# Kernel optimization log

Measured on AMD Instinct MI355X. Metric: run time of the kernel, lower is better.

## Reference

```python
import jax, jax.numpy as jnp
import numpy as np

N = 100000      # nodes
E = 1600000     # edges
D_IN = 128
D_H = 128
D_OUT = 128


def setup_inputs() -> dict:
    key = jax.random.key(0)
    k1, k2, k3, k4, k5, k6 = jax.random.split(key, 6)
    x = jax.random.normal(k1, (N, D_IN), dtype=jnp.float32)
    edge_index = jax.random.randint(k2, (2, E), 0, N, dtype=jnp.int32)
    # GCNConv params: glorot-ish scaled weights, zero bias (PyG default zeros bias)
    W1 = jax.random.normal(k3, (D_IN, D_H), dtype=jnp.float32) * (1.0 / np.sqrt(D_IN))
    b1 = jnp.zeros((D_H,), dtype=jnp.float32)
    W2 = jax.random.normal(k4, (D_H, D_OUT), dtype=jnp.float32) * (1.0 / np.sqrt(D_H))
    b2 = jnpps = jnp.zeros((D_OUT,), dtype=jnp.float32)
    return {"x": x, "edge_index": edge_index, "W1": W1, "b1": b1, "W2": W2, "b2": b2}


def _gcn_layer(x, edge_index, W, b):
    # PyG GCNConv with add_self_loops=True, symmetric normalization:
    # out = D^{-1/2} (A + I) D^{-1/2} (x W) + b, deg computed at target (col)
    n = x.shape[0]
    row, col = edge_index[0], edge_index[1]
    deg = jax.ops.segment_sum(jnp.ones(row.shape, dtype=x.dtype), col,
                              num_segments=n) + 1.0  # +1 for self-loop
    dinv = jax.lax.rsqrt(deg)                         # [N]
    h = x @ W                                         # [N, D_out]
    coef = dinv[row] * dinv[col]                      # [E]
    agg = jax.ops.segment_sum(h[row] * coef[:, None], col, num_segments=n)
    agg = agg + (dinv * dinv)[:, None] * h            # self-loop term
    return agg + b


def reference(x, edge_index, W1, b1, W2, b2):
    h = jax.nn.relu(_gcn_layer(x, edge_index, W1, b1))
    return _gcn_layer(h, edge_index, W2, b2)
```

## Files before the change

### kernel.cpp

```cpp
#include <hip/hip_runtime.h>
#include <hip/hip_bf16.h>

using bf16 = __hip_bfloat16;
typedef __attribute__((ext_vector_type(8))) short short8;
typedef __attribute__((ext_vector_type(4))) float floatx4;
typedef __attribute__((ext_vector_type(4))) unsigned int uint4v;
typedef __attribute__((ext_vector_type(4))) float float4v;

__device__ __forceinline__ float bf2f(unsigned int u) {
    union { unsigned int i; float f; } x; x.i = u << 16; return x.f;
}
__device__ __forceinline__ float bf2f_hi(unsigned int u) {
    union { unsigned int i; float f; } x; x.i = u & 0xffff0000u; return x.f;
}
__device__ __forceinline__ unsigned short f2bf(float f) {
    union { float f; unsigned int i; } x; x.f = f;
    unsigned int r = x.i + 0x7fffu + ((x.i >> 16) & 1u);
    return (unsigned short)(r >> 16);
}

#define TSHIFT 9
#define TNODES 512
#define NCHUNK 8192
#define EPT 32

__global__ __launch_bounds__(256)
void prep_w(const float* __restrict__ W1, const float* __restrict__ W2,
            unsigned short* __restrict__ Wt, unsigned int* __restrict__ sent,
            int* __restrict__ tileCur, int T) {
    if (blockIdx.x == 0 && threadIdx.x < 64) sent[threadIdx.x] = 0u;
    if (blockIdx.x == 1 && threadIdx.x < T) tileCur[threadIdx.x] = 0;
    const int id = blockIdx.x * 256 + threadIdx.x;
    const int m = id >> 14;
    const int r = id & 16383;
    const int n = r >> 7, k = r & 127;
    const float* W = m ? W2 : W1;
    Wt[((size_t)m << 14) + n * 128 + k] = f2bf(W[(size_t)k * 128 + n]);
}

__global__ __launch_bounds__(256)
void scatter_tiles(const int* __restrict__ row, const int* __restrict__ col,
                   int* __restrict__ tileCur, int* __restrict__ tileBuf,
                   int E, int T, int tcap) {
    __shared__ int grouped[NCHUNK];
    __shared__ int cnt[256], lo[256], off[256], lcur[256];
    const int t = threadIdx.x;
    const int e0 = blockIdx.x * NCHUNK;
    const int valid = min(NCHUNK, E - e0);
    cnt[t] = 0; lcur[t] = 0;
    int cc[EPT];
    #pragma unroll
    for (int k = 0; k < EPT; ++k) {
        int i = t + k * 256;
        cc[k] = (i < valid) ? col[e0 + i] : -1;
    }
    __syncthreads();
    #pragma unroll
    for (int k = 0; k < EPT; ++k)
        if (cc[k] >= 0) atomicAdd(&cnt[(unsigned)cc[k] >> TSHIFT], 1);
    __syncthreads();
    if (t == 0) {
        int run = 0;
        for (int s = 0; s < T; ++s) { lo[s] = run; run += cnt[s]; }
    }
    __syncthreads();
    if (t < T) off[t] = atomicAdd(&tileCur[t], cnt[t]);
    #pragma unroll
    for (int k = 0; k < EPT; ++k) {
        if (cc[k] >= 0) {
            int c = cc[k];
            int tl = (unsigned)c >> TSHIFT;
            int slot = lo[tl] + atomicAdd(&lcur[tl], 1);
            grouped[slot] = ((c & (TNODES - 1)) << 17) | row[e0 + t + k * 256];
        }
    }
    __syncthreads();
    for (int i = t; i < valid; i += 256) {
        int a = 0, b = T - 1;
        while (a < b) { int m = (a + b + 1) >> 1; if (lo[m] <= i) a = m; else b = m - 1; }
        tileBuf[(size_t)a * tcap + off[a] + (i - lo[a])] = grouped[i];
    }
}

__global__ __launch_bounds__(512)
void build_csr(const int* __restrict__ tileCur, const int* __restrict__ tileBuf,
               int* __restrict__ csr, int* __restrict__ rowptr,
               int* __restrict__ deg64, float* __restrict__ dinv,
               int N, int tcap) {
    __shared__ int deg[TNODES];
    __shared__ int offs[TNODES];
    __shared__ int tsum[TNODES];
    const int t = threadIdx.x;
    const int tile = blockIdx.x;
    const int nbase = tile << TSHIFT;
    const int cnt = tileCur[tile];
    const int* buf = tileBuf + (size_t)tile * tcap;
    deg[t] = 0;
    __syncthreads();
    for (int i = t; i < cnt; i += 512)
        atomicAdd(&deg[buf[i] >> 17], 1);
    __syncthreads();
    const int a0 = deg[t];
    tsum[t] = a0;
    __syncthreads();
    #pragma unroll
    for (int d = 1; d < 512; d <<= 1) {
        int v = (t >= d) ? tsum[t - d] : 0;
        __syncthreads();
        tsum[t] += v;
        __syncthreads();
    }
    const int tb = tsum[t] - a0;
    offs[t] = tb;
    const size_t gbase = (size_t)tile * tcap;
    const int node = nbase + t;
    if (node < N) {
        rowptr[node] = (int)(gbase + tb);
        deg64[node] = min(a0, 64);
        dinv[node] = rsqrtf((float)a0 + 1.0f);
    }
    deg[t] = 0;
    __syncthreads();
    for (int i = t; i < cnt; i += 512) {
        int p = buf[i];
        int ln = p >> 17;
        int pos = offs[ln] + atomicAdd(&deg[ln], 1);
        csr[gbase + pos] = p & 0x1FFFF;
    }
}

template <bool RELU, typename OutT>
__global__ __launch_bounds__(256)
void aggregate(const bf16* __restrict__ xin, const float* __restrict__ dinv,
               const int* __restrict__ deg64, const int* __restrict__ rowptr,
               const int* __restrict__ csr,
               const float* __restrict__ bias, OutT* __restrict__ aggout,
               int n) {
    const int wave = (blockIdx.x * blockDim.x + threadIdx.x) >> 6;
    const int lane = threadIdx.x & 63;
    if (wave >= n) return;
    const int c = wave;

    const int dg = deg64[c];
    const int base = rowptr[c];
    int idx = n;
    if (lane < dg)
        idx = __builtin_nontemporal_load(&csr[base + lane]);

    const int q = lane >> 4;
    const int s = lane & 15;
    const unsigned short* xq = (const unsigned short*)xin + s * 8;

    float acc[8] = {};
    for (int i = 0; i < dg; i += 16) {
        #pragma unroll
        for (int j = 0; j < 4; ++j) {
            const int e = i + 4 * j + q;
            const int se = __shfl(idx, e, 64);
            uint4 u = *reinterpret_cast<const uint4*>(xq + (size_t)se * 128);
            acc[0] += bf2f(u.x & 0xffffu); acc[1] += bf2f_hi(u.x);
            acc[2] += bf2f(u.y & 0xffffu); acc[3] += bf2f_hi(u.y);
            acc[4] += bf2f(u.z & 0xffffu); acc[5] += bf2f_hi(u.z);
            acc[6] += bf2f(u.w & 0xffffu); acc[7] += bf2f_hi(u.w);
        }
    }
    #pragma unroll
    for (int d = 0; d < 8; ++d) {
        acc[d] += __shfl(acc[d], lane ^ 16, 64);
        acc[d] += __shfl(acc[d], lane ^ 32, 64);
    }

    if (lane < 16) {
        const float wc = dinv[c];
        uint4 uc = *reinterpret_cast<const uint4*>(xq + (size_t)c * 128);
        float sf[8] = { bf2f(uc.x & 0xffffu), bf2f_hi(uc.x),
                        bf2f(uc.y & 0xffffu), bf2f_hi(uc.y),
                        bf2f(uc.z & 0xffffu), bf2f_hi(uc.z),
                        bf2f(uc.w & 0xffffu), bf2f_hi(uc.w) };
        const float4* bb4 = reinterpret_cast<const float4*>(bias + s * 8);
        float4 b0 = bb4[0], b1 = bb4[1];
        float r[8];
        r[0] = (acc[0] + sf[0]) * wc + b0.x;
        r[1] = (acc[1] + sf[1]) * wc + b0.y;
        r[2] = (acc[2] + sf[2]) * wc + b0.z;
        r[3] = (acc[3] + sf[3]) * wc + b0.w;
        r[4] = (acc[4] + sf[4]) * wc + b1.x;
        r[5] = (acc[5] + sf[5]) * wc + b1.y;
        r[6] = (acc[6] + sf[6]) * wc + b1.z;
        r[7] = (acc[7] + sf[7]) * wc + b1.w;
        if (RELU) {
            #pragma unroll
            for (int d = 0; d < 8; ++d) r[d] = fmaxf(r[d], 0.f);
        }
        if constexpr (sizeof(OutT) == 2) {
            uint4v u;
            u.x = ((unsigned)f2bf(r[1]) << 16) | f2bf(r[0]);
            u.y = ((unsigned)f2bf(r[3]) << 16) | f2bf(r[2]);
            u.z = ((unsigned)f2bf(r[5]) << 16) | f2bf(r[4]);
            u.w = ((unsigned)f2bf(r[7]) << 16) | f2bf(r[6]);
            __builtin_nontemporal_store(u,
                (uint4v*)((unsigned short*)aggout + (size_t)c * 128 + s * 8));
        } else {
            float4v v0 = { r[0], r[1], r[2], r[3] };
            float4v v1 = { r[4], r[5], r[6], r[7] };
            float4v* dst = (float4v*)((float*)aggout + (size_t)c * 128 + s * 8);
            __builtin_nontemporal_store(v0, dst);
            __builtin_nontemporal_store(v1, dst + 1);
        }
    }
}

#define WSTR 168
template <typename AT>
__launch_bounds__(256)
__global__ void gemm_mfma(const AT* __restrict__ A, const unsigned short* __restrict__ Wt,
                          const float* __restrict__ dinv,
                          bf16* __restrict__ out, int M) {
    __shared__ unsigned short sWt[128 * WSTR];
    const int t = threadIdx.x;
    const int row0 = blockIdx.x * 64;
    const int wv = t >> 6;
    const int L  = t & 63;
    const int q  = L >> 4;
    const int l16 = L & 15;
    const int myrow = row0 + wv * 16 + l16;

    short8 af[4];
    if constexpr (sizeof(AT) == 4) {
        const bool ok = myrow < M;
        const float* Af = (const float*)A + (size_t)myrow * 128 + q * 8;
        #pragma unroll
        for (int c = 0; c < 4; ++c) {
            float4 v0 = make_float4(0.f, 0.f, 0.f, 0.f);
            float4 v1 = make_float4(0.f, 0.f, 0.f, 0.f);
            if (ok) {
                v0 = *reinterpret_cast<const float4*>(Af + c * 32);
                v1 = *reinterpret_cast<const float4*>(Af + c * 32 + 4);
            }
            af[c][0] = (short)f2bf(v0.x); af[c][1] = (short)f2bf(v0.y);
            af[c][2] = (short)f2bf(v0.z); af[c][3] = (short)f2bf(v0.w);
            af[c][4] = (short)f2bf(v1.x); af[c][5] = (short)f2bf(v1.y);
            af[c][6] = (short)f2bf(v1.z); af[c][7] = (short)f2bf(v1.w);
        }
    } else {
        const int ridx = myrow < M ? myrow : M;
        const unsigned short* Ab = (const unsigned short*)A + (size_t)ridx * 128 + q * 8;
        #pragma unroll
        for (int c = 0; c < 4; ++c)
            af[c] = *reinterpret_cast<const short8*>(Ab + c * 32);
    }

    #pragma unroll
    for (int i = 0; i < 8; ++i) {
        int s = t + 256 * i;
        int nn = s >> 4, k0 = (s & 15) * 8;
        *reinterpret_cast<uint4*>(&sWt[nn * WSTR + k0]) =
            *reinterpret_cast<const uint4*>(&Wt[(size_t)nn * 128 + k0]);
    }
    __syncthreads();

    floatx4 acc[8] = {};
    #pragma unroll
    for (int c = 0; c < 4; ++c) {
        #pragma unroll
        for (int nt = 0; nt < 8; ++nt) {
            short8 b = *reinterpret_cast<const short8*>(&sWt[(nt * 16 + l16) * WSTR + c * 32 + q * 8]);
            acc[nt] = __builtin_amdgcn_mfma_f32_16x16x32_bf16(af[c], b, acc[nt], 0, 0, 0);
        }
    }

    float dv[4];
    #pragma unroll
    for (int i = 0; i < 4; ++i) {
        int r = wv * 16 + q * 4 + i;
        dv[i] = (row0 + r < M) ? dinv[row0 + r] : 1.f;
    }
    __syncthreads();
    unsigned short* sOut = sWt;
    #pragma unroll
    for (int nt = 0; nt < 8; ++nt) {
        #pragma unroll
        for (int i = 0; i < 4; ++i) {
            int r = wv * 16 + q * 4 + i;
            sOut[r * 128 + nt * 16 + l16] = f2bf(acc[nt][i] * dv[i]);
        }
    }
    __syncthreads();
    #pragma unroll
    for (int i = 0; i < 4; ++i) {
        int idx = t + 256 * i;
        int r = idx >> 4, c8 = (idx & 15) * 8;
        if (row0 + r < M)
            *reinterpret_cast<uint4*>(out + (size_t)(row0 + r) * 128 + c8) =
                *reinterpret_cast<const uint4*>(&sOut[r * 128 + c8]);
    }
}

extern "C" void kernel_launch(void* const* d_in, const int* in_sizes, int n_in,
                              void* d_out, int out_size, void* d_ws, size_t ws_size,
                              hipStream_t stream) {
    const float* x  = (const float*)d_in[0];
    const int*   ei = (const int*)d_in[1];
    const float* W1 = (const float*)d_in[2];
    const float* b1 = (const float*)d_in[3];
    const float* W2 = (const float*)d_in[4];
    const float* b2 = (const float*)d_in[5];
    float* out = (float*)d_out;

    const int N = in_sizes[0] / 128;
    const int E = in_sizes[1] / 2;
    const int* row = ei;
    const int* col = ei + E;

    const int T = (N + TNODES - 1) >> TSHIFT;
    const int meanT = (E + T - 1) / T;
    const int tcap = meanT + meanT / 8 + 1024;

    char* ws = (char*)d_ws;
    size_t off = 0;
    auto alloc = [&](size_t bytes) {
        void* p = ws + off;
        off += (bytes + 255) & ~(size_t)255;
        return p;
    };
    int*   tileCur = (int*)alloc((size_t)T * 4);
    int*   tileBuf = (int*)alloc((size_t)T * tcap * 4);
    int*   csr     = (int*)alloc((size_t)T * tcap * 4);
    int*   rowptr  = (int*)alloc((size_t)N * 4);
    int*   deg64   = (int*)alloc((size_t)N * 4);
    float* dinv    = (float*)alloc((size_t)N * 4);
    unsigned short* Wt = (unsigned short*)alloc(2 * 16384 * 2);
    bf16*  ha_bf   = (bf16*)alloc((size_t)(N + 1) * 128 * 2);
    bf16*  h1_bf   = (bf16*)alloc((size_t)(N + 1) * 128 * 2);

    prep_w<<<128, 256, 0, stream>>>(W1, W2, Wt,
                                    (unsigned int*)(ha_bf + (size_t)N * 128),
                                    tileCur, T);
    hipMemsetAsync(h1_bf + (size_t)N * 128, 0, 256, stream);
    scatter_tiles<<<(E + NCHUNK - 1) / NCHUNK, 256, 0, stream>>>(
        row, col, tileCur, tileBuf, E, T, tcap);
    build_csr<<<T, TNODES, 0, stream>>>(tileCur, tileBuf, csr, rowptr,
                                        deg64, dinv, N, tcap);

    const int aggBlocks = (int)(((size_t)N * 64 + 255) / 256);
    const int gemmBlocks = (N + 63) / 64;

    gemm_mfma<float><<<gemmBlocks, 256, 0, stream>>>(x, Wt, dinv, ha_bf, N);
    aggregate<true, bf16><<<aggBlocks, 256, 0, stream>>>(ha_bf, dinv, deg64, rowptr, csr, b1, h1_bf, N);

    gemm_mfma<bf16><<<gemmBlocks, 256, 0, stream>>>(h1_bf, Wt + 16384, dinv, ha_bf, N);
    aggregate<false, float><<<aggBlocks, 256, 0, stream>>>(ha_bf, dinv, deg64, rowptr, csr, b2, out, N);
}
```

Measured before the change: 313.0 us.

## Streamline CSR build: register-cached edges, wave-shuffle scan, drop memset and binary search

Several preprocessing tweaks land together. scatter_tiles halves its chunk size and records each slot's tile id in shared memory, which removes the per-element binary search. build_csr keeps the tile's edges in registers (up to KMAX per thread) instead of reading them twice, and replaces the barrier-heavy shared-memory scan with wave shuffles plus per-wave partials. The h1 sentinel memset is folded into prep_w, saving one stream operation. The risk is that tcap is now clamped to KMAX*512, so a tile with more edges than that would overflow or be dropped, and the register array adds pressure.

```diff
diff --git a/kernel.cpp b/kernel.cpp
--- a/kernel.cpp
+++ b/kernel.cpp
@@ -21,14 +21,16 @@
 
 #define TSHIFT 9
 #define TNODES 512
-#define NCHUNK 8192
-#define EPT 32
+#define NCHUNK 4096
+#define EPT 16
+#define KMAX 24
 
 __global__ __launch_bounds__(256)
 void prep_w(const float* __restrict__ W1, const float* __restrict__ W2,
-            unsigned short* __restrict__ Wt, unsigned int* __restrict__ sent,
-            int* __restrict__ tileCur, int T) {
-    if (blockIdx.x == 0 && threadIdx.x < 64) sent[threadIdx.x] = 0u;
+            unsigned short* __restrict__ Wt, unsigned int* __restrict__ sent1,
+            unsigned int* __restrict__ sent2, int* __restrict__ tileCur, int T) {
+    if (blockIdx.x == 0 && threadIdx.x < 64) sent1[threadIdx.x] = 0u;
+    if (blockIdx.x == 2 && threadIdx.x < 64) sent2[threadIdx.x] = 0u;
     if (blockIdx.x == 1 && threadIdx.x < T) tileCur[threadIdx.x] = 0;
     const int id = blockIdx.x * 256 + threadIdx.x;
     const int m = id >> 14;
@@ -43,6 +45,7 @@
                    int* __restrict__ tileCur, int* __restrict__ tileBuf,
                    int E, int T, int tcap) {
     __shared__ int grouped[NCHUNK];
+    __shared__ unsigned short tlOf[NCHUNK];
     __shared__ int cnt[256], lo[256], off[256], lcur[256];
     const int t = threadIdx.x;
     const int e0 = blockIdx.x * NCHUNK;
@@ -72,13 +75,13 @@
             int tl = (unsigned)c >> TSHIFT;
             int slot = lo[tl] + atomicAdd(&lcur[tl], 1);
             grouped[slot] = ((c & (TNODES - 1)) << 17) | row[e0 + t + k * 256];
+            tlOf[slot] = (unsigned short)tl;
         }
     }
     __syncthreads();
     for (int i = t; i < valid; i += 256) {
-        int a = 0, b = T - 1;
-        while (a < b) { int m = (a + b + 1) >> 1; if (lo[m] <= i) a = m; else b = m - 1; }
-        tileBuf[(size_t)a * tcap + off[a] + (i - lo[a])] = grouped[i];
+        int tl = tlOf[i];
+        tileBuf[(size_t)tl * tcap + off[tl] + (i - lo[tl])] = grouped[i];
     }
 }
 
@@ -89,28 +92,39 @@
                int N, int tcap) {
     __shared__ int deg[TNODES];
     __shared__ int offs[TNODES];
-    __shared__ int tsum[TNODES];
+    __shared__ int wpart[8];
     const int t = threadIdx.x;
+    const int lane = t & 63, w = t >> 6;
     const int tile = blockIdx.x;
     const int nbase = tile << TSHIFT;
     const int cnt = tileCur[tile];
     const int* buf = tileBuf + (size_t)tile * tcap;
     deg[t] = 0;
     __syncthreads();
-    for (int i = t; i < cnt; i += 512)
-        atomicAdd(&deg[buf[i] >> 17], 1);
+    int pv[KMAX];
+    #pragma unroll
+    for (int k = 0; k < KMAX; ++k) {
+        int i = t + k * 512;
+        pv[k] = (i < cnt) ? buf[i] : -1;
+    }
+    #pragma unroll
+    for (int k = 0; k < KMAX; ++k)
+        if (pv[k] >= 0) atomicAdd(&deg[pv[k] >> 17], 1);
     __syncthreads();
     const int a0 = deg[t];
-    tsum[t] = a0;
-    __syncthreads();
-    #pragma unroll
-    for (int d = 1; d < 512; d <<= 1) {
-        int v = (t >= d) ? tsum[t - d] : 0;
-        __syncthreads();
-        tsum[t] += v;
-        __syncthreads();
-    }
-    const int tb = tsum[t] - a0;
+    int v = a0;
+    #pragma unroll
+    for (int d = 1; d < 64; d <<= 1) {
+        int o = __shfl_up(v, d, 64);
+        if (lane >= d) v += o;
+    }
+    if (lane == 63) wpart[w] = v;
+    __syncthreads();
+    int basev = 0;
+    #pragma unroll
+    for (int j = 0; j < 8; ++j)
+        if (j < w) basev += wpart[j];
+    const int tb = basev + v - a0;
     offs[t] = tb;
     const size_t gbase = (size_t)tile * tcap;
     const int node = nbase + t;
@@ -121,11 +135,13 @@
     }
     deg[t] = 0;
     __syncthreads();
-    for (int i = t; i < cnt; i += 512) {
-        int p = buf[i];
-        int ln = p >> 17;
-        int pos = offs[ln] + atomicAdd(&deg[ln], 1);
-        csr[gbase + pos] = p & 0x1FFFF;
+    #pragma unroll
+    for (int k = 0; k < KMAX; ++k) {
+        if (pv[k] >= 0) {
+            int ln = pv[k] >> 17;
+            int pos = offs[ln] + atomicAdd(&deg[ln], 1);
+            csr[gbase + pos] = pv[k] & 0x1FFFF;
+        }
     }
 }
 
@@ -314,7 +330,8 @@
 
     const int T = (N + TNODES - 1) >> TSHIFT;
     const int meanT = (E + T - 1) / T;
-    const int tcap = meanT + meanT / 8 + 1024;
+    int tcap = meanT + meanT / 8 + 1024;
+    if (tcap > KMAX * TNODES) tcap = KMAX * TNODES;
 
     char* ws = (char*)d_ws;
     size_t off = 0;
@@ -335,8 +352,8 @@
 
     prep_w<<<128, 256, 0, stream>>>(W1, W2, Wt,
                                     (unsigned int*)(ha_bf + (size_t)N * 128),
+                                    (unsigned int*)(h1_bf + (size_t)N * 128),
                                     tileCur, T);
-    hipMemsetAsync(h1_bf + (size_t)N * 128, 0, 256, stream);
     scatter_tiles<<<(E + NCHUNK - 1) / NCHUNK, 256, 0, stream>>>(
         row, col, tileCur, tileBuf, E, T, tcap);
     build_csr<<<T, TNODES, 0, stream>>>(tileCur, tileBuf, csr, rowptr,
```

After: 289.7 us. 7.5% less time.
